# Optimization experiments

Measured on AMD Instinct MI355X. Metric: run time of the kernel, lower is better.

The kernel has to match this reference:

```python
import jax, jax.numpy as jnp
import numpy as np
from jax import lax

B, H, L, N, COUT = 16, 128, 8192, 16, 128
NEG_SLOPE = 0.3
BN_EPS = 1e-5


def setup_inputs() -> dict:
    key = jax.random.key(0)
    ks = jax.random.split(key, 20)
    x = jax.random.normal(ks[0], (B, H, L), dtype=jnp.float32)
    # --- S4D parameters ---
    log_dt = jnp.log(0.001) + jax.random.uniform(ks[1], (H,), dtype=jnp.float32) * (jnp.log(0.1) - jnp.log(0.001))
    A_log = jnp.log(0.5 * jnp.ones((H, N), dtype=jnp.float32))  # real part magnitude
    A_imag = jnp.broadcast_to(np.pi * jnp.arange(N, dtype=jnp.float32), (H, N)).copy()
    B_re = jnp.ones((H, N), dtype=jnp.float32)
    B_im = jnp.zeros((H, N), dtype=jnp.float32)
    C_re = jax.random.normal(ks[2], (H, N), dtype=jnp.float32) * (0.5 ** 0.5)
    C_im = jax.random.normal(ks[3], (H, N), dtype=jnp.float32) * (0.5 ** 0.5)
    D = jax.random.normal(ks[4], (H,), dtype=jnp.float32)
    # --- dilated conv branches (kernel_size=3, stride=4) ---
    wscale = 1.0 / np.sqrt(H * 3)
    w1 = jax.random.normal(ks[5], (COUT, H, 3), dtype=jnp.float32) * wscale
    b1 = jnp.zeros((COUT,), dtype=jnp.float32)
    w2 = jax.random.normal(ks[6], (COUT, H, 3), dtype=jnp.float32) * wscale
    b2 = jnp.zeros((COUT,), dtype=jnp.float32)
    w3 = jax.random.normal(ks[7], (COUT, H, 3), dtype=jnp.float32) * wscale
    b3 = jnp.zeros((COUT,), dtype=jnp.float32)
    w4 = jax.random.normal(ks[8], (COUT, H, 3), dtype=jnp.float32) * wscale
    b4 = jnp.zeros((COUT,), dtype=jnp.float32)
    gamma = jnp.ones((COUT,), dtype=jnp.float32)
    beta = jnp.zeros((COUT,), dtype=jnp.float32)
    return dict(x=x, log_dt=log_dt, A_log=A_log, A_imag=A_imag, B_re=B_re, B_im=B_im,
                C_re=C_re, C_im=C_im, D=D, w1=w1, b1=b1, w2=w2, b2=b2, w3=w3, b3=b3,
                w4=w4, b4=b4, gamma=gamma, beta=beta)


def _s4d(x, log_dt, A_log, A_imag, B_re, B_im, C_re, C_im, D):
    # x: (B,H,L). S4D with ZOH discretization, FFT long convolution.
    Lx = x.shape[-1]
    dt = jnp.exp(log_dt)[:, None]                    # (H,1)
    A = -jnp.exp(A_log) + 1j * A_imag                # (H,N)
    dtA = dt * A                                     # (H,N)
    dB = (jnp.exp(dtA) - 1.0) / A * (B_re + 1j * B_im)
    CB = (C_re + 1j * C_im) * dB                     # (H,N)
    l = jnp.arange(Lx, dtype=jnp.float32)
    vand = jnp.exp(dtA[:, :, None] * l)              # (H,N,L) Vandermonde
    K = 2.0 * jnp.real(jnp.einsum('hn,hnl->hl', CB, vand))  # (H,L)
    n = 2 * Lx
    Uf = jnp.fft.rfft(x, n=n)                        # (B,H,L+1)
    Kf = jnp.fft.rfft(K, n=n)                        # (H,L+1)
    y = jnp.fft.irfft(Uf * Kf, n=n)[..., :Lx]
    return y + D[:, None] * x


def _dconv(x, w, b, dil, pad):
    y = lax.conv_general_dilated(x, w, window_strides=(4,), padding=[(pad, pad)],
                                 rhs_dilation=(dil,), dimension_numbers=('NCH', 'OIH', 'NCH'))
    return y + b[:, None]


def _bn(z, gamma, beta):
    # training-mode BatchNorm1d: batch stats over (B, L_out) per channel
    m = jnp.mean(z, axis=(0, 2), keepdims=True)
    v = jnp.var(z, axis=(0, 2), keepdims=True)
    return gamma[:, None] * (z - m) * lax.rsqrt(v + BN_EPS) + beta[:, None]


def _lrelu(z):
    return jnp.where(z >= 0, z, NEG_SLOPE * z)


def reference(x, log_dt, A_log, A_imag, B_re, B_im, C_re, C_im, D,
              w1, b1, w2, b2, w3, b3, w4, b4, gamma, beta):
    y = _s4d(x, log_dt, A_log, A_imag, B_re, B_im, C_re, C_im, D)
    d1 = _bn(_dconv(y, w1, b1, 1, 1), gamma, beta)                 # no activation on branch 1
    d2 = _bn(_lrelu(_dconv(y, w2, b2, 2, 2)), gamma, beta)
    d3 = _bn(_lrelu(_dconv(y, w3, b3, 4, 4)), gamma, beta)
    d4 = _bn(_lrelu(_dconv(y, w4, b4, 8, 8)), gamma, beta)
    return jnp.concatenate([d1, d2, d3, d4], axis=1)               # (B, 4*COUT, L//4)
```

## Files before the change

kernel.cpp:

```cpp
#include <hip/hip_runtime.h>
#include <math.h>

typedef unsigned short u16x8 __attribute__((ext_vector_type(8)));
typedef unsigned short u16x2 __attribute__((ext_vector_type(2)));
typedef short s16x8 __attribute__((ext_vector_type(8)));
typedef float f32x4 __attribute__((ext_vector_type(4)));

__device__ __forceinline__ float bf2f(unsigned short u) {
    union { unsigned int i; float f; } v; v.i = ((unsigned int)u) << 16; return v.f;
}
__device__ __forceinline__ unsigned short f2bf(float f) {
    union { unsigned int i; float f; } v; v.f = f;
    unsigned int r = v.i + 0x7FFFu + ((v.i >> 16) & 1u);
    return (unsigned short)(r >> 16);
}

#define MATS_OFF 16384
#define WB_OFF   548864
#define STAT_OFF 942080
#define Y_OFF    1048576
#define YT_OFF   34603008
#define Z_OFF    Y_OFF

__global__ void precompute_s4d(const float* __restrict__ log_dt,
                               const float* __restrict__ A_log,
                               const float* __restrict__ A_imag,
                               const float* __restrict__ B_re,
                               const float* __restrict__ B_im,
                               const float* __restrict__ C_re,
                               const float* __restrict__ C_im,
                               float* __restrict__ w32,
                               unsigned short* __restrict__ MATS)
{
    const int h = blockIdx.x;
    const int tid = threadIdx.x;
    const double dt = exp((double)log_dt[h]);

    #pragma unroll 1
    for (int it = 0; it < 4; it++) {
        int idx = tid + (it << 8);
        int s = idx >> 5, i = idx & 31;
        int n = s >> 1;
        double Ar = -exp((double)A_log[h * 16 + n]);
        double Ai = (double)A_imag[h * 16 + n];
        double dr = dt * Ar, di = dt * Ai;
        double l = (double)(31 - i);
        double e = exp(l * dr);
        double val = (s & 1) ? e * sin(l * di) : e * cos(l * di);
        MATS[(size_t)h * 2080 + s * 32 + i] = f2bf((float)val);
    }
    #pragma unroll 1
    for (int it = 0; it < 4; it++) {
        int idx = tid + (it << 8);
        int j = idx >> 5, s = idx & 31;
        int n = s >> 1;
        double Ar = -exp((double)A_log[h * 16 + n]);
        double Ai = (double)A_imag[h * 16 + n];
        double dr = dt * Ar, di = dt * Ai;
        double ew = exp(dr);
        double wr = ew * cos(di), wi = ew * sin(di);
        double nr = wr - 1.0, ni = wi;
        double inv = 1.0 / (Ar * Ar + Ai * Ai);
        double tr = (nr * Ar + ni * Ai) * inv;
        double ti = (ni * Ar - nr * Ai) * inv;
        double Br = (double)B_re[h * 16 + n], Bi = (double)B_im[h * 16 + n];
        double dbr = tr * Br - ti * Bi, dbi = tr * Bi + ti * Br;
        double Cr = (double)C_re[h * 16 + n], Ci = (double)C_im[h * 16 + n];
        double cbr = Cr * dbr - Ci * dbi, cbi = Cr * dbi + Ci * dbr;
        double m = (double)(j + 1);
        double e = exp(m * dr);
        double pr = e * cos(m * di), pi = e * sin(m * di);
        double gr = cbr * pr - cbi * pi, gi = cbr * pi + cbi * pr;
        double val = (s & 1) ? -2.0 * gi : 2.0 * gr;
        MATS[(size_t)h * 2080 + 1024 + j * 32 + s] = f2bf((float)val);
    }
    {
        int l = tid >> 3, sub = tid & 7;
        double accd = 0.0;
        #pragma unroll 1
        for (int q = 0; q < 2; q++) {
            int n = sub * 2 + q;
            double Ar = -exp((double)A_log[h * 16 + n]);
            double Ai = (double)A_imag[h * 16 + n];
            double dr = dt * Ar, di = dt * Ai;
            double ew = exp(dr);
            double wr = ew * cos(di), wi = ew * sin(di);
            double nr = wr - 1.0, ni = wi;
            double inv = 1.0 / (Ar * Ar + Ai * Ai);
            double tr = (nr * Ar + ni * Ai) * inv;
            double ti = (ni * Ar - nr * Ai) * inv;
            double Br = (double)B_re[h * 16 + n], Bi = (double)B_im[h * 16 + n];
            double dbr = tr * Br - ti * Bi, dbi = tr * Bi + ti * Br;
            double Cr = (double)C_re[h * 16 + n], Ci = (double)C_im[h * 16 + n];
            double cbr = Cr * dbr - Ci * dbi, cbi = Cr * dbi + Ci * dbr;
            double l2 = (double)l;
            double e = exp(l2 * dr);
            double wlr = e * cos(l2 * di), wli = e * sin(l2 * di);
            accd += cbr * wlr - cbi * wli;
        }
        float accf = (float)(2.0 * accd);
        #pragma unroll
        for (int o = 4; o > 0; o >>= 1) accf += __shfl_down(accf, o, 8);
        if (sub == 0) MATS[(size_t)h * 2080 + 2048 + l] = f2bf(accf);
    }
    if (tid < 16) {
        int n = tid;
        double Ar = -exp((double)A_log[h * 16 + n]);
        double Ai = (double)A_imag[h * 16 + n];
        double dr = dt * Ar, di = dt * Ai;
        double e = exp(32.0 * dr);
        w32[h * 32 + 2 * n]     = (float)(e * cos(32.0 * di));
        w32[h * 32 + 2 * n + 1] = (float)(e * sin(32.0 * di));
    }
}

__global__ void wpack(const float* __restrict__ w1, const float* __restrict__ w2,
                      const float* __restrict__ w3, const float* __restrict__ w4,
                      unsigned short* __restrict__ WB)
{
    int idx = blockIdx.x * 256 + threadIdx.x;
    int br = idx / 49152;
    int r  = idx - br * 49152;
    int co = r / 384;
    int k  = r - co * 384;
    int tap = k >> 7, h = k & 127;
    const float* wp = (br == 0) ? w1 : (br == 1) ? w2 : (br == 2) ? w3 : w4;
    WB[idx] = f2bf(wp[co * 384 + h * 3 + tap]);
}

__global__ __launch_bounds__(256, 2) void s4d_mfma(const float* __restrict__ x,
                                                   const float* __restrict__ w32,
                                                   const unsigned short* __restrict__ MATS,
                                                   const float* __restrict__ Dp,
                                                   unsigned short* __restrict__ yout)
{
    __shared__ unsigned short sXc[256 * 40];
    __shared__ unsigned short sM[3840];
    __shared__ float spow2[256];
    __shared__ unsigned short skr[32];
    __shared__ float swc[128];
    __shared__ float scratch[8320];
    const int tid = threadIdx.x;
    const int bh = blockIdx.x;
    const int h = bh & 127;
    const int lane = tid & 63, w = tid >> 6;
    const int ml = lane & 15, kg = lane >> 4;

    float xr[32];
    const float4* xp4 = (const float4*)(x + ((size_t)bh << 13) + (tid << 5));
    #pragma unroll
    for (int i = 0; i < 8; i++) {
        float4 v = xp4[i];
        xr[4 * i] = v.x; xr[4 * i + 1] = v.y; xr[4 * i + 2] = v.z; xr[4 * i + 3] = v.w;
    }
    #pragma unroll
    for (int g = 0; g < 4; g++) {
        u16x8 pk;
        #pragma unroll
        for (int e = 0; e < 8; e++) pk[e] = f2bf(xr[g * 8 + e]);
        *(u16x8*)&sXc[tid * 40 + g * 8] = pk;
    }
    {
        int matv = tid >> 7, r = (tid >> 2) & 31, sg = tid & 3;
        u16x8 v = *(const u16x8*)(MATS + (size_t)h * 2080 + matv * 1024 + r * 32 + sg * 8);
        *(u16x8*)&sM[matv * 2560 + r * 40 + sg * 8] = v;
    }
    if (tid < 4) {
        u16x8 v = *(const u16x8*)(MATS + (size_t)h * 2080 + 2048 + tid * 8);
        *(u16x8*)&skr[tid * 8] = v;
    }
    if (tid < 16) {
        float rr = w32[h * 32 + 2 * tid], ii = w32[h * 32 + 2 * tid + 1];
        #pragma unroll
        for (int k = 0; k < 8; k++) {
            spow2[k * 32 + 2 * tid] = rr; spow2[k * 32 + 2 * tid + 1] = ii;
            float n2r = rr * rr - ii * ii, n2i = 2.f * rr * ii;
            rr = n2r; ii = n2i;
        }
    }
    __syncthreads();
    #pragma unroll
    for (int it = 0; it < 4; it++) {
        int idx = tid + (it << 8);
        int j = idx >> 5, i = idx & 31;
        sM[1280 + j * 40 + i] = (i <= j) ? skr[j - i] : (unsigned short)0;
    }
    __syncthreads();

    f32x4 acc[2][4];
    #pragma unroll
    for (int mt = 0; mt < 2; mt++)
        #pragma unroll
        for (int nt = 0; nt < 4; nt++) acc[mt][nt] = (f32x4)(0.f);
    {
        s16x8 af[2], bfr[4];
        #pragma unroll
        for (int mt = 0; mt < 2; mt++)
            af[mt] = *(const s16x8*)&sM[(mt * 16 + ml) * 40 + kg * 8];
        #pragma unroll
        for (int nt = 0; nt < 4; nt++)
            bfr[nt] = *(const s16x8*)&sXc[(w * 64 + nt * 16 + ml) * 40 + kg * 8];
        #pragma unroll
        for (int mt = 0; mt < 2; mt++)
            #pragma unroll
            for (int nt = 0; nt < 4; nt++)
                acc[mt][nt] = __builtin_amdgcn_mfma_f32_16x16x32_bf16(af[mt], bfr[nt], acc[mt][nt], 0, 0, 0);
    }
    #pragma unroll
    for (int mt = 0; mt < 2; mt++)
        #pragma unroll
        for (int nt = 0; nt < 4; nt++)
            #pragma unroll
            for (int r = 0; r < 4; r++)
                scratch[(mt * 16 + kg * 4 + r) * 260 + (w * 64 + nt * 16 + ml)] = acc[mt][nt][r];
    __syncthreads();
    float zr[16], zi[16];
    #pragma unroll
    for (int n = 0; n < 16; n++) {
        zr[n] = scratch[(2 * n) * 260 + tid];
        zi[n] = scratch[(2 * n + 1) * 260 + tid];
    }

    #pragma unroll 1
    for (int k = 0; k < 6; k++) {
        const int o = 1 << k;
        const bool act = lane >= o;
        #pragma unroll
        for (int n = 0; n < 16; n++) {
            float lr = __shfl(zr[n], lane - o);
            float li = __shfl(zi[n], lane - o);
            float mr = spow2[(k << 5) + 2 * n], mi = spow2[(k << 5) + 2 * n + 1];
            float nzr = fmaf(mr, lr, fmaf(-mi, li, zr[n]));
            float nzi = fmaf(mr, li, fmaf(mi, lr, zi[n]));
            zr[n] = act ? nzr : zr[n];
            zi[n] = act ? nzi : zi[n];
        }
    }
    if (lane == 63) {
        #pragma unroll
        for (int n = 0; n < 16; n++) {
            swc[w * 32 + 2 * n]     = zr[n];
            swc[w * 32 + 2 * n + 1] = zi[n];
        }
    }
    __syncthreads();
    float qr[16], qi[16];
    #pragma unroll
    for (int n = 0; n < 16; n++) { qr[n] = 0.f; qi[n] = 0.f; }
    #pragma unroll 1
    for (int a = 0; a < 3; a++) {
        if (a < w) {
            int p = w - 1 - a;
            #pragma unroll
            for (int n = 0; n < 16; n++) {
                float ar = swc[a * 32 + 2 * n], ai = swc[a * 32 + 2 * n + 1];
                float mr = 1.f, mi = 0.f;
                if (p > 0) { mr = spow2[((5 + p) << 5) + 2 * n]; mi = spow2[((5 + p) << 5) + 2 * n + 1]; }
                qr[n] = fmaf(mr, ar, fmaf(-mi, ai, qr[n]));
                qi[n] = fmaf(mr, ai, fmaf(mi, ar, qi[n]));
            }
        }
    }
    float pjr[16], pji[16];
    #pragma unroll
    for (int n = 0; n < 16; n++) { pjr[n] = 1.f; pji[n] = 0.f; }
    #pragma unroll 1
    for (int k = 0; k < 6; k++) {
        const bool bit = (lane >> k) & 1;
        #pragma unroll
        for (int n = 0; n < 16; n++) {
            float mr = spow2[(k << 5) + 2 * n], mi = spow2[(k << 5) + 2 * n + 1];
            float nr2 = pjr[n] * mr - pji[n] * mi;
            float ni2 = fmaf(pjr[n], mi, pji[n] * mr);
            pjr[n] = bit ? nr2 : pjr[n];
            pji[n] = bit ? ni2 : pji[n];
        }
    }
    #pragma unroll
    for (int n = 0; n < 16; n++) {
        float pr = __shfl(zr[n], lane - 1);
        float pi = __shfl(zi[n], lane - 1);
        pr = (lane == 0) ? 0.f : pr;
        pi = (lane == 0) ? 0.f : pi;
        zr[n] = fmaf(pjr[n], qr[n], fmaf(-pji[n], qi[n], pr));
        zi[n] = fmaf(pjr[n], qi[n], fmaf(pji[n], qr[n], pi));
    }
    {
        unsigned short* sCc = (unsigned short*)scratch;
        #pragma unroll
        for (int g = 0; g < 4; g++) {
            u16x8 pk;
            #pragma unroll
            for (int q = 0; q < 4; q++) {
                pk[2 * q]     = f2bf(zr[g * 4 + q]);
                pk[2 * q + 1] = f2bf(zi[g * 4 + q]);
            }
            *(u16x8*)&sCc[tid * 40 + g * 8] = pk;
        }
    }
    __syncthreads();

    #pragma unroll
    for (int mt = 0; mt < 2; mt++)
        #pragma unroll
        for (int nt = 0; nt < 4; nt++) acc[mt][nt] = (f32x4)(0.f);
    {
        const unsigned short* sCc = (const unsigned short*)scratch;
        s16x8 a1[2], a2[2], bfx[4], bfc[4];
        #pragma unroll
        for (int mt = 0; mt < 2; mt++) {
            a1[mt] = *(const s16x8*)&sM[1280 + (mt * 16 + ml) * 40 + kg * 8];
            a2[mt] = *(const s16x8*)&sM[2560 + (mt * 16 + ml) * 40 + kg * 8];
        }
        #pragma unroll
        for (int nt = 0; nt < 4; nt++) {
            bfx[nt] = *(const s16x8*)&sXc[(w * 64 + nt * 16 + ml) * 40 + kg * 8];
            bfc[nt] = *(const s16x8*)&sCc[(w * 64 + nt * 16 + ml) * 40 + kg * 8];
        }
        #pragma unroll
        for (int mt = 0; mt < 2; mt++)
            #pragma unroll
            for (int nt = 0; nt < 4; nt++) {
                acc[mt][nt] = __builtin_amdgcn_mfma_f32_16x16x32_bf16(a1[mt], bfx[nt], acc[mt][nt], 0, 0, 0);
                acc[mt][nt] = __builtin_amdgcn_mfma_f32_16x16x32_bf16(a2[mt], bfc[nt], acc[mt][nt], 0, 0, 0);
            }
    }
    __syncthreads();
    #pragma unroll
    for (int mt = 0; mt < 2; mt++)
        #pragma unroll
        for (int nt = 0; nt < 4; nt++)
            #pragma unroll
            for (int r = 0; r < 4; r++)
                scratch[(mt * 16 + kg * 4 + r) * 260 + (w * 64 + nt * 16 + ml)] = acc[mt][nt][r];
    __syncthreads();
    const float Dh = Dp[h];
    u16x8* yp = (u16x8*)(yout + ((size_t)bh << 13) + (tid << 5));
    #pragma unroll
    for (int g = 0; g < 4; g++) {
        u16x8 pk;
        #pragma unroll
        for (int e = 0; e < 8; e++) {
            int i = g * 8 + e;
            pk[e] = f2bf(fmaf(Dh, xr[i], scratch[i * 260 + tid]));
        }
        yp[g] = pk;
    }
}

__global__ __launch_bounds__(256) void ytrans(const unsigned short* __restrict__ y,
                                              unsigned short* __restrict__ yT)
{
    __shared__ unsigned short sT[128 * 72];
    const int b = blockIdx.y, g0 = blockIdx.x << 6;
    const int tid = threadIdx.x;
    #pragma unroll
    for (int j = 0; j < 4; j++) {
        int li = tid + (j << 8);
        int h = li >> 3, g8 = (li & 7) << 3;
        u16x8 v = *(const u16x8*)(y + (((size_t)(b * 128 + h)) << 13) + g0 + g8);
        int gp = (g8 + (((h >> 3) & 7) << 3)) & 63;
        *(u16x8*)&sT[h * 72 + gp] = v;
    }
    __syncthreads();
    #pragma unroll
    for (int j = 0; j < 4; j++) {
        int li = tid + (j << 8);
        int g = li >> 4, h8 = (li & 15) << 3;
        u16x8 o;
        #pragma unroll
        for (int e = 0; e < 8; e++) {
            int h = h8 + e;
            int gp = (g + (((h >> 3) & 7) << 3)) & 63;
            o[e] = sT[h * 72 + gp];
        }
        *(u16x8*)(yT + (((size_t)(b * 8192 + g0 + g)) << 7) + h8) = o;
    }
}

__global__ __launch_bounds__(256) void conv_mfma(
    const unsigned short* __restrict__ yT,
    const unsigned short* __restrict__ WB,
    const float* __restrict__ b1, const float* __restrict__ b2,
    const float* __restrict__ b3, const float* __restrict__ b4,
    unsigned short* __restrict__ z)
{
    __shared__ unsigned short sW[128 * 40];
    __shared__ unsigned short sY[128 * 40];
    const int tid = threadIdx.x;
    const int lane = tid & 63, w = tid >> 6;
    const int branch = blockIdx.y, b = blockIdx.z;
    const int t0 = blockIdx.x << 7;
    const int d = 1 << branch;
    const int coH = (w & 1) << 6, tH = (w >> 1) << 6;
    const int ml = lane & 15, kg = lane >> 4;

    f32x4 acc[4][4];
    #pragma unroll
    for (int mt = 0; mt < 4; mt++)
        #pragma unroll
        for (int nt = 0; nt < 4; nt++) acc[mt][nt] = (f32x4)(0.f);

    const unsigned short* WBb = WB + (size_t)branch * 49152;

    for (int kc = 0; kc < 12; kc++) {
        const int tap = kc >> 2, hc = (kc & 3) << 5;
        const int goff = d * (tap - 1);
        __syncthreads();
        #pragma unroll
        for (int j = 0; j < 2; j++) {
            int li = tid + (j << 8);
            int co = li >> 2, kq = (li & 3) << 3;
            u16x8 v = *(const u16x8*)(WBb + (size_t)co * 384 + (kc << 5) + kq);
            *(u16x8*)&sW[co * 40 + kq] = v;
        }
        #pragma unroll
        for (int j = 0; j < 2; j++) {
            int li = tid + (j << 8);
            int n = li >> 2, kq = (li & 3) << 3;
            int g = ((t0 + n) << 2) + goff;
            u16x8 v;
            if ((unsigned)g < 8192u) {
                v = *(const u16x8*)(yT + (((size_t)(b * 8192 + g)) << 7) + hc + kq);
            } else {
                #pragma unroll
                for (int e = 0; e < 8; e++) v[e] = 0;
            }
            *(u16x8*)&sY[n * 40 + kq] = v;
        }
        __syncthreads();
        s16x8 af[4], bfr[4];
        #pragma unroll
        for (int mt = 0; mt < 4; mt++)
            af[mt] = *(const s16x8*)&sW[(coH + mt * 16 + ml) * 40 + (kg << 3)];
        #pragma unroll
        for (int nt = 0; nt < 4; nt++)
            bfr[nt] = *(const s16x8*)&sY[(tH + nt * 16 + ml) * 40 + (kg << 3)];
        #pragma unroll
        for (int mt = 0; mt < 4; mt++)
            #pragma unroll
            for (int nt = 0; nt < 4; nt++)
                acc[mt][nt] = __builtin_amdgcn_mfma_f32_16x16x32_bf16(af[mt], bfr[nt], acc[mt][nt], 0, 0, 0);
    }

    const float* bp = (branch == 0) ? b1 : (branch == 1) ? b2 : (branch == 2) ? b3 : b4;
    #pragma unroll
    for (int mt = 0; mt < 4; mt++) {
        #pragma unroll
        for (int r = 0; r < 4; r++) {
            const int co = coH + mt * 16 + (kg << 2) + r;
            const float bb = bp[co];
            #pragma unroll
            for (int nt = 0; nt < 4; nt++) {
                const int t = t0 + tH + nt * 16 + ml;
                float v = acc[mt][nt][r] + bb;
                if (branch != 0) v = (v >= 0.f) ? v : 0.3f * v;
                z[(((size_t)((branch * 16 + b) * 128 + co)) << 11) + t] = f2bf(v);
            }
        }
    }
}

__global__ __launch_bounds__(256) void bn_stats(const unsigned short* __restrict__ z,
                                                float* __restrict__ stats)
{
    const int bc = blockIdx.x;
    const int branch = bc >> 7, co = bc & 127;
    const int tid = threadIdx.x;
    float s1 = 0.f, s2 = 0.f;
    for (int i = tid; i < 16384; i += 256) {
        int b = i >> 10, tp = (i & 1023) << 1;
        const unsigned short* p = z + (((size_t)((branch * 16 + b) * 128 + co)) << 11) + tp;
        u16x2 v2 = *(const u16x2*)p;
        float a = bf2f(v2[0]), c = bf2f(v2[1]);
        s1 += a + c;
        s2 = fmaf(a, a, fmaf(c, c, s2));
    }
    #pragma unroll
    for (int o = 32; o > 0; o >>= 1) { s1 += __shfl_down(s1, o); s2 += __shfl_down(s2, o); }
    __shared__ float r1[4], r2[4];
    const int lane = tid & 63, wid = tid >> 6;
    if (lane == 0) { r1[wid] = s1; r2[wid] = s2; }
    __syncthreads();
    if (tid == 0) {
        float t1 = r1[0] + r1[1] + r1[2] + r1[3];
        float t2 = r2[0] + r2[1] + r2[2] + r2[3];
        float m = t1 * (1.0f / 32768.0f);
        float var = t2 * (1.0f / 32768.0f) - m * m;
        stats[bc * 2]     = m;
        stats[bc * 2 + 1] = 1.0f / sqrtf(var + 1e-5f);
    }
}

__global__ __launch_bounds__(256) void bn_apply(const unsigned short* __restrict__ z,
                                                const float* __restrict__ stats,
                                                const float* __restrict__ gam,
                                                const float* __restrict__ bet,
                                                float* __restrict__ out)
{
    const size_t idx = (((size_t)blockIdx.x << 8) + threadIdx.x) << 3;
    const int t = (int)(idx & 2047);
    const size_t bc = idx >> 11;
    const int ch = (int)(bc & 511);
    const int b = (int)(bc >> 9);
    const int branch = ch >> 7, co = ch & 127;
    const float m = stats[ch * 2], inv = stats[ch * 2 + 1];
    const float ga = gam[co], be = bet[co];
    const float sc = ga * inv, sh = fmaf(-m, sc, be);
    const unsigned short* zp = z + (((size_t)((branch * 16 + b) * 128 + co)) << 11) + t;
    u16x8 v = *(const u16x8*)zp;
    float4 o0, o1;
    o0.x = fmaf(bf2f(v[0]), sc, sh); o0.y = fmaf(bf2f(v[1]), sc, sh);
    o0.z = fmaf(bf2f(v[2]), sc, sh); o0.w = fmaf(bf2f(v[3]), sc, sh);
    o1.x = fmaf(bf2f(v[4]), sc, sh); o1.y = fmaf(bf2f(v[5]), sc, sh);
    o1.z = fmaf(bf2f(v[6]), sc, sh); o1.w = fmaf(bf2f(v[7]), sc, sh);
    *(float4*)(out + idx)     = o0;
    *(float4*)(out + idx + 4) = o1;
}

extern "C" void kernel_launch(void* const* d_in, const int* in_sizes, int n_in,
                              void* d_out, int out_size, void* d_ws, size_t ws_size,
                              hipStream_t stream) {
    const float* x      = (const float*)d_in[0];
    const float* log_dt = (const float*)d_in[1];
    const float* A_log  = (const float*)d_in[2];
    const float* A_imag = (const float*)d_in[3];
    const float* B_re   = (const float*)d_in[4];
    const float* B_im   = (const float*)d_in[5];
    const float* C_re   = (const float*)d_in[6];
    const float* C_im   = (const float*)d_in[7];
    const float* Dp     = (const float*)d_in[8];
    const float* w1 = (const float*)d_in[9];
    const float* b1 = (const float*)d_in[10];
    const float* w2 = (const float*)d_in[11];
    const float* b2 = (const float*)d_in[12];
    const float* w3 = (const float*)d_in[13];
    const float* b3 = (const float*)d_in[14];
    const float* w4 = (const float*)d_in[15];
    const float* b4 = (const float*)d_in[16];
    const float* gam = (const float*)d_in[17];
    const float* bet = (const float*)d_in[18];

    float* w32p = (float*)d_ws;
    unsigned short* MATSp = (unsigned short*)((char*)d_ws + MATS_OFF);
    unsigned short* WBp = (unsigned short*)((char*)d_ws + WB_OFF);
    float* stats = (float*)((char*)d_ws + STAT_OFF);
    unsigned short* yws = (unsigned short*)((char*)d_ws + Y_OFF);
    unsigned short* yT  = (unsigned short*)((char*)d_ws + YT_OFF);
    unsigned short* zws = (unsigned short*)((char*)d_ws + Z_OFF);
    float* out = (float*)d_out;

    precompute_s4d<<<dim3(128), dim3(256), 0, stream>>>(log_dt, A_log, A_imag,
                                                        B_re, B_im, C_re, C_im, w32p, MATSp);
    wpack<<<dim3(768), dim3(256), 0, stream>>>(w1, w2, w3, w4, WBp);
    s4d_mfma<<<dim3(2048), dim3(256), 0, stream>>>(x, w32p, MATSp, Dp, yws);
    ytrans<<<dim3(128, 16), dim3(256), 0, stream>>>(yws, yT);
    conv_mfma<<<dim3(16, 4, 16), dim3(256), 0, stream>>>(yT, WBp, b1, b2, b3, b4, zws);
    bn_stats<<<dim3(512), dim3(256), 0, stream>>>(zws, stats);
    bn_apply<<<dim3(8192), dim3(256), 0, stream>>>(zws, stats, gam, bet, out);
}
```

Measured before the change: 279.9 us.

## Precompute chunk powers, halve scratch LDS, raise s4d occupancy, split precompute grid

Splits the S4D parameter precompute across three blocks per head so its serial double-precision work runs in parallel. Adds a kernel that tabulates the powers w^(32l) per head into the yT workspace, which is free until ytrans runs. The main kernel now loads these powers instead of building them with a six-step binary-exponent multiply chain. The scratch staging is done in two halves so the shared buffer shrinks, allowing launch bounds of 3 blocks per SM, at the cost of extra barriers and more register pressure from holding the power arrays.

```diff
diff --git a/kernel.cpp b/kernel.cpp
--- a/kernel.cpp
+++ b/kernel.cpp
@@ -33,53 +33,30 @@
                                unsigned short* __restrict__ MATS)
 {
     const int h = blockIdx.x;
+    const int part = blockIdx.y;
     const int tid = threadIdx.x;
     const double dt = exp((double)log_dt[h]);
 
-    #pragma unroll 1
-    for (int it = 0; it < 4; it++) {
-        int idx = tid + (it << 8);
-        int s = idx >> 5, i = idx & 31;
-        int n = s >> 1;
-        double Ar = -exp((double)A_log[h * 16 + n]);
-        double Ai = (double)A_imag[h * 16 + n];
-        double dr = dt * Ar, di = dt * Ai;
-        double l = (double)(31 - i);
-        double e = exp(l * dr);
-        double val = (s & 1) ? e * sin(l * di) : e * cos(l * di);
-        MATS[(size_t)h * 2080 + s * 32 + i] = f2bf((float)val);
-    }
-    #pragma unroll 1
-    for (int it = 0; it < 4; it++) {
-        int idx = tid + (it << 8);
-        int j = idx >> 5, s = idx & 31;
-        int n = s >> 1;
-        double Ar = -exp((double)A_log[h * 16 + n]);
-        double Ai = (double)A_imag[h * 16 + n];
-        double dr = dt * Ar, di = dt * Ai;
-        double ew = exp(dr);
-        double wr = ew * cos(di), wi = ew * sin(di);
-        double nr = wr - 1.0, ni = wi;
-        double inv = 1.0 / (Ar * Ar + Ai * Ai);
-        double tr = (nr * Ar + ni * Ai) * inv;
-        double ti = (ni * Ar - nr * Ai) * inv;
-        double Br = (double)B_re[h * 16 + n], Bi = (double)B_im[h * 16 + n];
-        double dbr = tr * Br - ti * Bi, dbi = tr * Bi + ti * Br;
-        double Cr = (double)C_re[h * 16 + n], Ci = (double)C_im[h * 16 + n];
-        double cbr = Cr * dbr - Ci * dbi, cbi = Cr * dbi + Ci * dbr;
-        double m = (double)(j + 1);
-        double e = exp(m * dr);
-        double pr = e * cos(m * di), pi = e * sin(m * di);
-        double gr = cbr * pr - cbi * pi, gi = cbr * pi + cbi * pr;
-        double val = (s & 1) ? -2.0 * gi : 2.0 * gr;
-        MATS[(size_t)h * 2080 + 1024 + j * 32 + s] = f2bf((float)val);
-    }
-    {
-        int l = tid >> 3, sub = tid & 7;
-        double accd = 0.0;
+    if (part == 0) {
         #pragma unroll 1
-        for (int q = 0; q < 2; q++) {
-            int n = sub * 2 + q;
+        for (int it = 0; it < 4; it++) {
+            int idx = tid + (it << 8);
+            int s = idx >> 5, i = idx & 31;
+            int n = s >> 1;
+            double Ar = -exp((double)A_log[h * 16 + n]);
+            double Ai = (double)A_imag[h * 16 + n];
+            double dr = dt * Ar, di = dt * Ai;
+            double l = (double)(31 - i);
+            double e = exp(l * dr);
+            double val = (s & 1) ? e * sin(l * di) : e * cos(l * di);
+            MATS[(size_t)h * 2080 + s * 32 + i] = f2bf((float)val);
+        }
+    } else if (part == 1) {
+        #pragma unroll 1
+        for (int it = 0; it < 4; it++) {
+            int idx = tid + (it << 8);
+            int j = idx >> 5, s = idx & 31;
+            int n = s >> 1;
             double Ar = -exp((double)A_log[h * 16 + n]);
             double Ai = (double)A_imag[h * 16 + n];
             double dr = dt * Ar, di = dt * Ai;
@@ -93,25 +70,69 @@
             double dbr = tr * Br - ti * Bi, dbi = tr * Bi + ti * Br;
             double Cr = (double)C_re[h * 16 + n], Ci = (double)C_im[h * 16 + n];
             double cbr = Cr * dbr - Ci * dbi, cbi = Cr * dbi + Ci * dbr;
-            double l2 = (double)l;
-            double e = exp(l2 * dr);
-            double wlr = e * cos(l2 * di), wli = e * sin(l2 * di);
-            accd += cbr * wlr - cbi * wli;
-        }
-        float accf = (float)(2.0 * accd);
-        #pragma unroll
-        for (int o = 4; o > 0; o >>= 1) accf += __shfl_down(accf, o, 8);
-        if (sub == 0) MATS[(size_t)h * 2080 + 2048 + l] = f2bf(accf);
-    }
-    if (tid < 16) {
-        int n = tid;
-        double Ar = -exp((double)A_log[h * 16 + n]);
-        double Ai = (double)A_imag[h * 16 + n];
-        double dr = dt * Ar, di = dt * Ai;
-        double e = exp(32.0 * dr);
-        w32[h * 32 + 2 * n]     = (float)(e * cos(32.0 * di));
-        w32[h * 32 + 2 * n + 1] = (float)(e * sin(32.0 * di));
-    }
+            double m = (double)(j + 1);
+            double e = exp(m * dr);
+            double pr = e * cos(m * di), pi = e * sin(m * di);
+            double gr = cbr * pr - cbi * pi, gi = cbr * pi + cbi * pr;
+            double val = (s & 1) ? -2.0 * gi : 2.0 * gr;
+            MATS[(size_t)h * 2080 + 1024 + j * 32 + s] = f2bf((float)val);
+        }
+    } else {
+        {
+            int l = tid >> 3, sub = tid & 7;
+            double accd = 0.0;
+            #pragma unroll 1
+            for (int q = 0; q < 2; q++) {
+                int n = sub * 2 + q;
+                double Ar = -exp((double)A_log[h * 16 + n]);
+                double Ai = (double)A_imag[h * 16 + n];
+                double dr = dt * Ar, di = dt * Ai;
+                double ew = exp(dr);
+                double wr = ew * cos(di), wi = ew * sin(di);
+                double nr = wr - 1.0, ni = wi;
+                double inv = 1.0 / (Ar * Ar + Ai * Ai);
+                double tr = (nr * Ar + ni * Ai) * inv;
+                double ti = (ni * Ar - nr * Ai) * inv;
+                double Br = (double)B_re[h * 16 + n], Bi = (double)B_im[h * 16 + n];
+                double dbr = tr * Br - ti * Bi, dbi = tr * Bi + ti * Br;
+                double Cr = (double)C_re[h * 16 + n], Ci = (double)C_im[h * 16 + n];
+                double cbr = Cr * dbr - Ci * dbi, cbi = Cr * dbi + Ci * dbr;
+                double l2 = (double)l;
+                double e = exp(l2 * dr);
+                double wlr = e * cos(l2 * di), wli = e * sin(l2 * di);
+                accd += cbr * wlr - cbi * wli;
+            }
+            float accf = (float)(2.0 * accd);
+            #pragma unroll
+            for (int o = 4; o > 0; o >>= 1) accf += __shfl_down(accf, o, 8);
+            if (sub == 0) MATS[(size_t)h * 2080 + 2048 + l] = f2bf(accf);
+        }
+        if (tid < 16) {
+            int n = tid;
+            double Ar = -exp((double)A_log[h * 16 + n]);
+            double Ai = (double)A_imag[h * 16 + n];
+            double dr = dt * Ar, di = dt * Ai;
+            double e = exp(32.0 * dr);
+            w32[h * 32 + 2 * n]     = (float)(e * cos(32.0 * di));
+            w32[h * 32 + 2 * n + 1] = (float)(e * sin(32.0 * di));
+        }
+    }
+}
+
+__global__ void wpow_k(const float* __restrict__ log_dt,
+                       const float* __restrict__ A_log,
+                       const float* __restrict__ A_imag,
+                       float* __restrict__ wpow)
+{
+    int idx = blockIdx.x * 256 + threadIdx.x;
+    int h = idx >> 10, r = idx & 1023, l = r >> 4, n = r & 15;
+    double dt = exp((double)log_dt[h]);
+    double Ar = -exp((double)A_log[h * 16 + n]);
+    double Ai = (double)A_imag[h * 16 + n];
+    double m = 32.0 * (double)l;
+    double e = exp(m * dt * Ar);
+    wpow[(size_t)idx * 2]     = (float)(e * cos(m * dt * Ai));
+    wpow[(size_t)idx * 2 + 1] = (float)(e * sin(m * dt * Ai));
 }
 
 __global__ void wpack(const float* __restrict__ w1, const float* __restrict__ w2,
@@ -128,8 +149,9 @@
     WB[idx] = f2bf(wp[co * 384 + h * 3 + tap]);
 }
 
-__global__ __launch_bounds__(256, 2) void s4d_mfma(const float* __restrict__ x,
+__global__ __launch_bounds__(256, 3) void s4d_mfma(const float* __restrict__ x,
                                                    const float* __restrict__ w32,
+                                                   const float* __restrict__ wpow,
                                                    const unsigned short* __restrict__ MATS,
                                                    const float* __restrict__ Dp,
                                                    unsigned short* __restrict__ yout)
@@ -139,7 +161,7 @@
     __shared__ float spow2[256];
     __shared__ unsigned short skr[32];
     __shared__ float swc[128];
-    __shared__ float scratch[8320];
+    __shared__ float scratch[5200];
     const int tid = threadIdx.x;
     const int bh = blockIdx.x;
     const int h = bh & 127;
@@ -153,6 +175,16 @@
         float4 v = xp4[i];
         xr[4 * i] = v.x; xr[4 * i + 1] = v.y; xr[4 * i + 2] = v.z; xr[4 * i + 3] = v.w;
     }
+    float wlr[16], wli[16];
+    {
+        const float4* wp4 = (const float4*)(wpow + (((size_t)((h << 6) + lane)) << 5));
+        #pragma unroll
+        for (int i = 0; i < 8; i++) {
+            float4 v = wp4[i];
+            wlr[2 * i] = v.x;     wli[2 * i] = v.y;
+            wlr[2 * i + 1] = v.z; wli[2 * i + 1] = v.w;
+        }
+    }
     #pragma unroll
     for (int g = 0; g < 4; g++) {
         u16x8 pk;
@@ -206,19 +238,21 @@
             for (int nt = 0; nt < 4; nt++)
                 acc[mt][nt] = __builtin_amdgcn_mfma_f32_16x16x32_bf16(af[mt], bfr[nt], acc[mt][nt], 0, 0, 0);
     }
-    #pragma unroll
-    for (int mt = 0; mt < 2; mt++)
+    float zr[16], zi[16];
+    #pragma unroll 1
+    for (int ph = 0; ph < 2; ph++) {
         #pragma unroll
         for (int nt = 0; nt < 4; nt++)
             #pragma unroll
             for (int r = 0; r < 4; r++)
-                scratch[(mt * 16 + kg * 4 + r) * 260 + (w * 64 + nt * 16 + ml)] = acc[mt][nt][r];
-    __syncthreads();
-    float zr[16], zi[16];
-    #pragma unroll
-    for (int n = 0; n < 16; n++) {
-        zr[n] = scratch[(2 * n) * 260 + tid];
-        zi[n] = scratch[(2 * n + 1) * 260 + tid];
+                scratch[(kg * 4 + r) * 260 + (w * 64 + nt * 16 + ml)] = acc[ph][nt][r];
+        __syncthreads();
+        #pragma unroll
+        for (int n = 0; n < 8; n++) {
+            zr[ph * 8 + n] = scratch[(2 * n) * 260 + tid];
+            zi[ph * 8 + n] = scratch[(2 * n + 1) * 260 + tid];
+        }
+        __syncthreads();
     }
 
     #pragma unroll 1
@@ -261,29 +295,14 @@
             }
         }
     }
-    float pjr[16], pji[16];
-    #pragma unroll
-    for (int n = 0; n < 16; n++) { pjr[n] = 1.f; pji[n] = 0.f; }
-    #pragma unroll 1
-    for (int k = 0; k < 6; k++) {
-        const bool bit = (lane >> k) & 1;
-        #pragma unroll
-        for (int n = 0; n < 16; n++) {
-            float mr = spow2[(k << 5) + 2 * n], mi = spow2[(k << 5) + 2 * n + 1];
-            float nr2 = pjr[n] * mr - pji[n] * mi;
-            float ni2 = fmaf(pjr[n], mi, pji[n] * mr);
-            pjr[n] = bit ? nr2 : pjr[n];
-            pji[n] = bit ? ni2 : pji[n];
-        }
-    }
     #pragma unroll
     for (int n = 0; n < 16; n++) {
         float pr = __shfl(zr[n], lane - 1);
         float pi = __shfl(zi[n], lane - 1);
         pr = (lane == 0) ? 0.f : pr;
         pi = (lane == 0) ? 0.f : pi;
-        zr[n] = fmaf(pjr[n], qr[n], fmaf(-pji[n], qi[n], pr));
-        zi[n] = fmaf(pjr[n], qi[n], fmaf(pji[n], qr[n], pi));
+        zr[n] = fmaf(wlr[n], qr[n], fmaf(-wli[n], qi[n], pr));
+        zi[n] = fmaf(wlr[n], qi[n], fmaf(wli[n], qr[n], pi));
     }
     {
         unsigned short* sCc = (unsigned short*)scratch;
@@ -325,26 +344,27 @@
                 acc[mt][nt] = __builtin_amdgcn_mfma_f32_16x16x32_bf16(a2[mt], bfc[nt], acc[mt][nt], 0, 0, 0);
             }
     }
-    __syncthreads();
-    #pragma unroll
-    for (int mt = 0; mt < 2; mt++)
+    const float Dh = Dp[h];
+    #pragma unroll 1
+    for (int ph = 0; ph < 2; ph++) {
+        __syncthreads();
         #pragma unroll
         for (int nt = 0; nt < 4; nt++)
             #pragma unroll
             for (int r = 0; r < 4; r++)
-                scratch[(mt * 16 + kg * 4 + r) * 260 + (w * 64 + nt * 16 + ml)] = acc[mt][nt][r];
-    __syncthreads();
-    const float Dh = Dp[h];
-    u16x8* yp = (u16x8*)(yout + ((size_t)bh << 13) + (tid << 5));
-    #pragma unroll
-    for (int g = 0; g < 4; g++) {
-        u16x8 pk;
-        #pragma unroll
-        for (int e = 0; e < 8; e++) {
-            int i = g * 8 + e;
-            pk[e] = f2bf(fmaf(Dh, xr[i], scratch[i * 260 + tid]));
-        }
-        yp[g] = pk;
+                scratch[(kg * 4 + r) * 260 + (w * 64 + nt * 16 + ml)] = acc[ph][nt][r];
+        __syncthreads();
+        u16x8* yp = (u16x8*)(yout + ((size_t)bh << 13) + (tid << 5) + (ph << 4));
+        #pragma unroll
+        for (int g = 0; g < 2; g++) {
+            u16x8 pk;
+            #pragma unroll
+            for (int e = 0; e < 8; e++) {
+                int i = (ph << 4) + (g << 3) + e;
+                pk[e] = f2bf(fmaf(Dh, xr[i], scratch[((g << 3) + e) * 260 + tid]));
+            }
+            yp[g] = pk;
+        }
     }
 }
 
@@ -547,13 +567,15 @@
     float* stats = (float*)((char*)d_ws + STAT_OFF);
     unsigned short* yws = (unsigned short*)((char*)d_ws + Y_OFF);
     unsigned short* yT  = (unsigned short*)((char*)d_ws + YT_OFF);
+    float* wpow = (float*)((char*)d_ws + YT_OFF);
     unsigned short* zws = (unsigned short*)((char*)d_ws + Z_OFF);
     float* out = (float*)d_out;
 
-    precompute_s4d<<<dim3(128), dim3(256), 0, stream>>>(log_dt, A_log, A_imag,
-                                                        B_re, B_im, C_re, C_im, w32p, MATSp);
+    precompute_s4d<<<dim3(128, 3), dim3(256), 0, stream>>>(log_dt, A_log, A_imag,
+                                                           B_re, B_im, C_re, C_im, w32p, MATSp);
+    wpow_k<<<dim3(512), dim3(256), 0, stream>>>(log_dt, A_log, A_imag, wpow);
     wpack<<<dim3(768), dim3(256), 0, stream>>>(w1, w2, w3, w4, WBp);
-    s4d_mfma<<<dim3(2048), dim3(256), 0, stream>>>(x, w32p, MATSp, Dp, yws);
+    s4d_mfma<<<dim3(2048), dim3(256), 0, stream>>>(x, w32p, wpow, MATSp, Dp, yws);
     ytrans<<<dim3(128, 16), dim3(256), 0, stream>>>(yws, yT);
     conv_mfma<<<dim3(16, 4, 16), dim3(256), 0, stream>>>(yT, WBp, b1, b2, b3, b4, zws);
     bn_stats<<<dim3(512), dim3(256), 0, stream>>>(zws, stats);
```

After: 372.1 us. 1.33x slower.
